# Optimization experiments

Hardware: AMD Instinct MI355X
Metric: run time of the kernel (lower is better)

Reference implementation:

```python
import jax, jax.numpy as jnp
import numpy as np

D = 50          # half-window
K = 2 * D + 1   # 101 window positions
P_SIZE = 100    # predictive-alignment hidden dim


def setup_inputs() -> dict:
    key = jax.random.key(0)
    ks = jax.random.split(key, 5)
    B, S, CQ, CC = 2, 2048, 256, 256
    q = jax.random.normal(ks[0], (B, S, CQ), jnp.float32)
    c_t = jax.random.normal(ks[1], (B, S, CC), jnp.float32)
    W_a = jax.random.normal(ks[2], (CC, CQ), jnp.float32) / np.sqrt(CQ).astype(np.float32)
    W_p = jax.random.normal(ks[3], (P_SIZE, CC), jnp.float32) / np.sqrt(CC).astype(np.float32)
    V_p = jax.random.normal(ks[4], (1, P_SIZE), jnp.float32) / np.sqrt(P_SIZE).astype(np.float32)
    return {"q": q, "c_t": c_t, "W_a": W_a, "W_p": W_p, "V_p": V_p}


def reference(q, c_t, W_a, W_p, V_p):
    B, S, CQ = q.shape
    # predictive alignment: p in (0, S), one predicted center per (b, s)
    p = S * jax.nn.sigmoid(jnp.tanh(c_t @ W_p.T) @ V_p.T)[..., 0]          # [B,S]
    offs = jnp.arange(-D, D + 1)                                           # [K]
    # torch .long() truncates toward zero (raw can be negative)
    raw = jnp.trunc(p[..., None] + offs[None, None, :] + 1.0).astype(jnp.int32)
    # clamp to [0, S+1] then mod (S+1): index 0 == padded (invalid) row,
    # matching torch's NaN-padded row 0 (S+1 wraps to 0 via the modulo)
    idx = jnp.clip(raw, 0, S + 1) % (S + 1)                                # [B,S,K]
    mask = idx == 0                                                        # invalid window slots
    # pad row 0 (torch pads with NaN then zeroes the NaN rows; we pad with 0
    # and mask by index -> identical math for finite q)
    q_pad = jnp.concatenate([jnp.zeros((B, 1, CQ), q.dtype), q], axis=1)   # [B,S+1,CQ]
    gathered = jnp.take_along_axis(q_pad, idx.reshape(B, S * K, 1), axis=1)
    q1 = jnp.where(mask[..., None], 0.0, gathered.reshape(B, S, K, CQ))    # [B,S,K,CQ]
    # score: W_a projection then dot with context
    Wq = jnp.einsum("bskq,cq->bskc", q1, W_a)                              # [B,S,K,CC]
    a = jnp.einsum("bskc,bsc->bsk", Wq, c_t)                               # [B,S,K]
    a = jnp.where(mask, -jnp.inf, a)
    attn = jax.nn.softmax(a, axis=2)                                       # [B,S,K]
    # gaussian decay centered at floor(p) (p > 0 so trunc == floor)
    exponent = -2.0 * (((offs[None, None, :] + jnp.trunc(p)[..., None] - p[..., None]) / D) ** 2)
    w = attn * jnp.exp(exponent)                                           # [B,S,K]
    s_t = jnp.einsum("bsk,bskc->bsc", w, q1)                               # [B,S,CQ]
    return s_t
```

## Files before the change

kernel.cpp:

```cpp
#include <hip/hip_runtime.h>
#include <math.h>

#define S_LEN 2048
#define NB    2
#define CQ_   256
#define CC_   256
#define DH    50
#define KW    101
#define PS    100
#define RB    8
#define HPAD  128
#define WTH   1e-5f

__global__ __launch_bounds__(128) void k_prep(const float* __restrict__ Wp,
                                              float* __restrict__ WpT) {
  const int c = blockIdx.x, j = threadIdx.x;
  WpT[c * HPAD + j] = (j < PS) ? Wp[j * CC_ + c] : 0.0f;
}

__global__ __launch_bounds__(384, 3) void k_align(const float* __restrict__ ct,
    const float* __restrict__ Wa, const float* __restrict__ WpT,
    const float* __restrict__ Vp, float* __restrict__ p_out,
    float* __restrict__ V_out) {
  const int r0  = blockIdx.x * RB;
  const int tid = threadIdx.x;
  const float* crow = ct + (size_t)r0 * CC_;

  __shared__ float red[RB][PS + 4];

  if (tid < CQ_) {
    const float* wa = Wa + tid;
    float acc[RB];
#pragma unroll
    for (int r = 0; r < RB; ++r) acc[r] = 0.0f;

    float4 cv0[RB], cv1[RB];
#pragma unroll
    for (int r = 0; r < RB; ++r) cv0[r] = *(const float4*)&crow[r * CC_];
    float w00 = wa[0 * CQ_], w01 = wa[1 * CQ_], w02 = wa[2 * CQ_], w03 = wa[3 * CQ_];

    for (int c = 0; c < CC_ - 4; c += 4) {
      const int cn = c + 4;
#pragma unroll
      for (int r = 0; r < RB; ++r) cv1[r] = *(const float4*)&crow[r * CC_ + cn];
      const float w10 = wa[(size_t)(cn + 0) * CQ_];
      const float w11 = wa[(size_t)(cn + 1) * CQ_];
      const float w12 = wa[(size_t)(cn + 2) * CQ_];
      const float w13 = wa[(size_t)(cn + 3) * CQ_];
#pragma unroll
      for (int r = 0; r < RB; ++r) {
        float t = acc[r];
        t = fmaf(cv0[r].x, w00, t);
        t = fmaf(cv0[r].y, w01, t);
        t = fmaf(cv0[r].z, w02, t);
        t = fmaf(cv0[r].w, w03, t);
        acc[r] = t;
      }
#pragma unroll
      for (int r = 0; r < RB; ++r) cv0[r] = cv1[r];
      w00 = w10; w01 = w11; w02 = w12; w03 = w13;
    }
#pragma unroll
    for (int r = 0; r < RB; ++r) {
      float t = acc[r];
      t = fmaf(cv0[r].x, w00, t);
      t = fmaf(cv0[r].y, w01, t);
      t = fmaf(cv0[r].z, w02, t);
      t = fmaf(cv0[r].w, w03, t);
      acc[r] = t;
    }
#pragma unroll
    for (int r = 0; r < RB; ++r)
      V_out[(size_t)(r0 + r) * CQ_ + tid] = acc[r];
  } else {
    const int j = tid - CQ_;
    const float* wh = WpT + j;
    float ah[RB];
#pragma unroll
    for (int r = 0; r < RB; ++r) ah[r] = 0.0f;

    float4 cv0[RB], cv1[RB];
#pragma unroll
    for (int r = 0; r < RB; ++r) cv0[r] = *(const float4*)&crow[r * CC_];
    float w00 = wh[0 * HPAD], w01 = wh[1 * HPAD], w02 = wh[2 * HPAD], w03 = wh[3 * HPAD];

    for (int c = 0; c < CC_ - 4; c += 4) {
      const int cn = c + 4;
#pragma unroll
      for (int r = 0; r < RB; ++r) cv1[r] = *(const float4*)&crow[r * CC_ + cn];
      const float w10 = wh[(size_t)(cn + 0) * HPAD];
      const float w11 = wh[(size_t)(cn + 1) * HPAD];
      const float w12 = wh[(size_t)(cn + 2) * HPAD];
      const float w13 = wh[(size_t)(cn + 3) * HPAD];
#pragma unroll
      for (int r = 0; r < RB; ++r) {
        float t = ah[r];
        t = fmaf(cv0[r].x, w00, t);
        t = fmaf(cv0[r].y, w01, t);
        t = fmaf(cv0[r].z, w02, t);
        t = fmaf(cv0[r].w, w03, t);
        ah[r] = t;
      }
#pragma unroll
      for (int r = 0; r < RB; ++r) cv0[r] = cv1[r];
      w00 = w10; w01 = w11; w02 = w12; w03 = w13;
    }
#pragma unroll
    for (int r = 0; r < RB; ++r) {
      float t = ah[r];
      t = fmaf(cv0[r].x, w00, t);
      t = fmaf(cv0[r].y, w01, t);
      t = fmaf(cv0[r].z, w02, t);
      t = fmaf(cv0[r].w, w03, t);
      ah[r] = t;
    }
    if (j < PS) {
      const float vp = Vp[j];
#pragma unroll
      for (int r = 0; r < RB; ++r) red[r][j] = vp * tanhf(ah[r]);
    }
  }
  __syncthreads();
  if (tid < RB) {
    float s = 0.0f;
    for (int j = 0; j < PS; ++j) s += red[tid][j];
    p_out[r0 + tid] = (float)S_LEN * (1.0f / (1.0f + expf(-s)));
  }
}

__global__ __launch_bounds__(256, 4) void k_attn(const float* __restrict__ q,
    const float* __restrict__ p_in, const float* V,
    float* out) {
  const int wid  = threadIdx.x >> 6;
  const int row  = (blockIdx.x << 2) + wid;
  const int lane = threadIdx.x & 63;
  const int b    = row >> 11;

  __shared__ float ss[4][128];
  __shared__ float sw[4][128];

  const float p  = p_in[row];
  const float tp = truncf(p);
  const float* qb = q + (size_t)b * S_LEN * CQ_;

  const int sub = lane >> 4;
  const int cb  = (lane & 15) * 16;

  const float* vrow = V + (size_t)row * CQ_ + cb;
  const float4 v0 = *(const float4*)(vrow);
  const float4 v1 = *(const float4*)(vrow + 4);
  const float4 v2 = *(const float4*)(vrow + 8);
  const float4 v3 = *(const float4*)(vrow + 12);

  if (lane >= KW - 64) ss[wid][64 + lane] = -INFINITY;

  for (int g = 0; g < 26; g += 2) {
    const int ka = (g << 2) + sub;
    const int kb = ka + 4;
    const float ta = p + (float)(ka - DH) + 1.0f;
    const float tb = p + (float)(kb - DH) + 1.0f;
    const int rawa = (int)ta;
    const int rawb = (int)tb;
    const bool oka = (rawa >= 1) && (rawa <= S_LEN) && (ka < KW);
    const bool okb = (rawb >= 1) && (rawb <= S_LEN) && (kb < KW);
    const float* qra = qb + (size_t)(oka ? rawa - 1 : 0) * CQ_ + cb;
    const float* qrb = qb + (size_t)(okb ? rawb - 1 : 0) * CQ_ + cb;

    const float4 a0 = *(const float4*)(qra);
    const float4 a1 = *(const float4*)(qra + 4);
    const float4 a2 = *(const float4*)(qra + 8);
    const float4 a3 = *(const float4*)(qra + 12);
    const float4 b0 = *(const float4*)(qrb);
    const float4 b1 = *(const float4*)(qrb + 4);
    const float4 b2 = *(const float4*)(qrb + 8);
    const float4 b3 = *(const float4*)(qrb + 12);

    float t0 = a0.x * v0.x, t1 = a1.x * v1.x, t2 = a2.x * v2.x, t3 = a3.x * v3.x;
    t0 = fmaf(a0.y, v0.y, t0); t1 = fmaf(a1.y, v1.y, t1);
    t2 = fmaf(a2.y, v2.y, t2); t3 = fmaf(a3.y, v3.y, t3);
    t0 = fmaf(a0.z, v0.z, t0); t1 = fmaf(a1.z, v1.z, t1);
    t2 = fmaf(a2.z, v2.z, t2); t3 = fmaf(a3.z, v3.z, t3);
    t0 = fmaf(a0.w, v0.w, t0); t1 = fmaf(a1.w, v1.w, t1);
    t2 = fmaf(a2.w, v2.w, t2); t3 = fmaf(a3.w, v3.w, t3);
    float sA = (t0 + t1) + (t2 + t3);
    sA += __shfl_xor(sA, 1, 64);
    sA += __shfl_xor(sA, 2, 64);
    sA += __shfl_xor(sA, 4, 64);
    sA += __shfl_xor(sA, 8, 64);
    sA = oka ? sA : -INFINITY;
    if ((lane & 15) == 0) ss[wid][ka] = sA;

    float u0 = b0.x * v0.x, u1 = b1.x * v1.x, u2 = b2.x * v2.x, u3 = b3.x * v3.x;
    u0 = fmaf(b0.y, v0.y, u0); u1 = fmaf(b1.y, v1.y, u1);
    u2 = fmaf(b2.y, v2.y, u2); u3 = fmaf(b3.y, v3.y, u3);
    u0 = fmaf(b0.z, v0.z, u0); u1 = fmaf(b1.z, v1.z, u1);
    u2 = fmaf(b2.z, v2.z, u2); u3 = fmaf(b3.z, v3.z, u3);
    u0 = fmaf(b0.w, v0.w, u0); u1 = fmaf(b1.w, v1.w, u1);
    u2 = fmaf(b2.w, v2.w, u2); u3 = fmaf(b3.w, v3.w, u3);
    float sB = (u0 + u1) + (u2 + u3);
    sB += __shfl_xor(sB, 1, 64);
    sB += __shfl_xor(sB, 2, 64);
    sB += __shfl_xor(sB, 4, 64);
    sB += __shfl_xor(sB, 8, 64);
    sB = okb ? sB : -INFINITY;
    if ((lane & 15) == 0) ss[wid][kb] = sB;
  }

  const float s0 = ss[wid][lane];
  const float s1 = ss[wid][64 + lane];

  float m = fmaxf(s0, s1);
#pragma unroll
  for (int off = 1; off < 64; off <<= 1) m = fmaxf(m, __shfl_xor(m, off, 64));

  const float e0 = __expf(s0 - m);
  const float e1 = __expf(s1 - m);
  float den = e0 + e1;
#pragma unroll
  for (int off = 1; off < 64; off <<= 1) den += __shfl_xor(den, off, 64);
  const float inv = 1.0f / den;

  float g0 = ((float)(lane - DH) + tp - p) / (float)DH;
  float g1 = ((float)(lane + (64 - DH)) + tp - p) / (float)DH;
  const float w0 = e0 * __expf(-2.0f * g0 * g0) * inv;
  const float w1 = e1 * __expf(-2.0f * g1 * g1) * inv;
  sw[wid][lane] = w0;
  if (lane < KW - 64) sw[wid][64 + lane] = w1;

  unsigned long long m0 = __ballot(w0 > WTH);
  unsigned long long m1 = __ballot((lane < KW - 64) && (w1 > WTH));

  float4 acc = make_float4(0.0f, 0.0f, 0.0f, 0.0f);
  while ((m0 | m1) != 0ull) {
    int kk[4];
#pragma unroll
    for (int i = 0; i < 4; ++i) {
      int k = -1;
      if (m0)      { k = __builtin_ctzll(m0);      m0 &= m0 - 1; }
      else if (m1) { k = 64 + __builtin_ctzll(m1); m1 &= m1 - 1; }
      kk[i] = k;
    }
#pragma unroll
    for (int i = 0; i < 4; ++i) {
      if (kk[i] >= 0) {
        const float wk = sw[wid][kk[i]];
        const float t = p + (float)(kk[i] - DH) + 1.0f;
        const int r = (int)t - 1;
        const float4 qv = *(const float4*)(qb + (size_t)r * CQ_ + lane * 4);
        acc.x = fmaf(wk, qv.x, acc.x);
        acc.y = fmaf(wk, qv.y, acc.y);
        acc.z = fmaf(wk, qv.z, acc.z);
        acc.w = fmaf(wk, qv.w, acc.w);
      }
    }
  }
  *(float4*)(out + (size_t)row * CQ_ + lane * 4) = acc;
}

extern "C" void kernel_launch(void* const* d_in, const int* in_sizes, int n_in,
                              void* d_out, int out_size, void* d_ws, size_t ws_size,
                              hipStream_t stream) {
  const float* q  = (const float*)d_in[0];
  const float* ct = (const float*)d_in[1];
  const float* Wa = (const float*)d_in[2];
  const float* Wp = (const float*)d_in[3];
  const float* Vp = (const float*)d_in[4];
  float* out = (float*)d_out;

  float* ws     = (float*)d_ws;
  float* p_ws   = ws;
  float* WpT_ws = ws + NB * S_LEN;

  k_prep <<<CC_, HPAD, 0, stream>>>(Wp, WpT_ws);
  k_align<<<(NB * S_LEN) / RB, 384, 0, stream>>>(ct, Wa, WpT_ws, Vp, p_ws, out);
  k_attn <<<(NB * S_LEN) / 4, 256, 0, stream>>>(q, p_ws, out, out);
}
```

Baseline: 120.1 us.

## Replace row-blocked align kernel with shared-memory tiled GEMM over concatenated weights

Concatenates W_a and W_p into one packed [CC,384] weight matrix and computes c_t times it with a classic 64x64 LDS-tiled SGEMM, writing both the W_a projection and the hidden pre-activations to a workspace buffer. A separate small kernel then applies tanh, the V_p dot and the sigmoid to produce p, and the attention kernel reads its projection from the wider workspace rows. The aim is much better weight reuse than the old per-8-row kernel, which reread the weights from global memory for every block. In exchange it adds an extra kernel launch and a G workspace write/read.

```diff
diff --git a/kernel.cpp b/kernel.cpp
--- a/kernel.cpp
+++ b/kernel.cpp
@@ -8,129 +8,100 @@
 #define DH    50
 #define KW    101
 #define PS    100
-#define RB    8
-#define HPAD  128
 #define WTH   1e-5f
 
-__global__ __launch_bounds__(128) void k_prep(const float* __restrict__ Wp,
-                                              float* __restrict__ WpT) {
-  const int c = blockIdx.x, j = threadIdx.x;
-  WpT[c * HPAD + j] = (j < PS) ? Wp[j * CC_ + c] : 0.0f;
-}
-
-__global__ __launch_bounds__(384, 3) void k_align(const float* __restrict__ ct,
-    const float* __restrict__ Wa, const float* __restrict__ WpT,
-    const float* __restrict__ Vp, float* __restrict__ p_out,
-    float* __restrict__ V_out) {
-  const int r0  = blockIdx.x * RB;
+#define NB2   384
+#define MT    64
+#define NT    64
+#define KC    32
+
+__global__ __launch_bounds__(NB2) void k_prep(const float* __restrict__ Wa,
+    const float* __restrict__ Wp, float* __restrict__ BT) {
+  const int c = blockIdx.x, n = threadIdx.x;
+  float v = 0.0f;
+  if (n < CQ_)            v = Wa[(size_t)c * CQ_ + n];
+  else if (n < CQ_ + PS)  v = Wp[(size_t)(n - CQ_) * CC_ + c];
+  BT[(size_t)c * NB2 + n] = v;
+}
+
+__global__ __launch_bounds__(256) void k_gemm(const float* __restrict__ ct,
+    const float* __restrict__ BT, float* __restrict__ G) {
+  const int bm = blockIdx.x & 63;
+  const int bn = blockIdx.x >> 6;
+  const int r0 = bm * MT;
+  const int n0 = bn * NT;
   const int tid = threadIdx.x;
-  const float* crow = ct + (size_t)r0 * CC_;
-
-  __shared__ float red[RB][PS + 4];
-
-  if (tid < CQ_) {
-    const float* wa = Wa + tid;
-    float acc[RB];
-#pragma unroll
-    for (int r = 0; r < RB; ++r) acc[r] = 0.0f;
-
-    float4 cv0[RB], cv1[RB];
-#pragma unroll
-    for (int r = 0; r < RB; ++r) cv0[r] = *(const float4*)&crow[r * CC_];
-    float w00 = wa[0 * CQ_], w01 = wa[1 * CQ_], w02 = wa[2 * CQ_], w03 = wa[3 * CQ_];
-
-    for (int c = 0; c < CC_ - 4; c += 4) {
-      const int cn = c + 4;
-#pragma unroll
-      for (int r = 0; r < RB; ++r) cv1[r] = *(const float4*)&crow[r * CC_ + cn];
-      const float w10 = wa[(size_t)(cn + 0) * CQ_];
-      const float w11 = wa[(size_t)(cn + 1) * CQ_];
-      const float w12 = wa[(size_t)(cn + 2) * CQ_];
-      const float w13 = wa[(size_t)(cn + 3) * CQ_];
-#pragma unroll
-      for (int r = 0; r < RB; ++r) {
-        float t = acc[r];
-        t = fmaf(cv0[r].x, w00, t);
-        t = fmaf(cv0[r].y, w01, t);
-        t = fmaf(cv0[r].z, w02, t);
-        t = fmaf(cv0[r].w, w03, t);
-        acc[r] = t;
-      }
-#pragma unroll
-      for (int r = 0; r < RB; ++r) cv0[r] = cv1[r];
-      w00 = w10; w01 = w11; w02 = w12; w03 = w13;
+  const int tx = tid & 15, ty = tid >> 4;
+
+  __shared__ float As[KC][MT + 4];
+  __shared__ float Bs[KC][NT + 4];
+
+  float acc[4][4];
+#pragma unroll
+  for (int i = 0; i < 4; ++i)
+#pragma unroll
+    for (int j = 0; j < 4; ++j) acc[i][j] = 0.0f;
+
+  const int kq = tid & 7,  mA = tid >> 3;
+  const int nq = tid & 15, kB = tid >> 4;
+
+  for (int c0 = 0; c0 < CC_; c0 += KC) {
+    const float4 a0 = *(const float4*)&ct[(size_t)(r0 + mA) * CC_ + c0 + kq * 4];
+    const float4 a1 = *(const float4*)&ct[(size_t)(r0 + mA + 32) * CC_ + c0 + kq * 4];
+    const float4 b0 = *(const float4*)&BT[(size_t)(c0 + kB) * NB2 + n0 + nq * 4];
+    const float4 b1 = *(const float4*)&BT[(size_t)(c0 + kB + 16) * NB2 + n0 + nq * 4];
+    __syncthreads();
+    As[kq * 4 + 0][mA] = a0.x;
+    As[kq * 4 + 1][mA] = a0.y;
+    As[kq * 4 + 2][mA] = a0.z;
+    As[kq * 4 + 3][mA] = a0.w;
+    As[kq * 4 + 0][mA + 32] = a1.x;
+    As[kq * 4 + 1][mA + 32] = a1.y;
+    As[kq * 4 + 2][mA + 32] = a1.z;
+    As[kq * 4 + 3][mA + 32] = a1.w;
+    *(float4*)&Bs[kB][nq * 4]      = b0;
+    *(float4*)&Bs[kB + 16][nq * 4] = b1;
+    __syncthreads();
+#pragma unroll
+    for (int k = 0; k < KC; ++k) {
+      const float4 av = *(const float4*)&As[k][ty * 4];
+      const float4 bv = *(const float4*)&Bs[k][tx * 4];
+      const float a[4] = {av.x, av.y, av.z, av.w};
+      const float b[4] = {bv.x, bv.y, bv.z, bv.w};
+#pragma unroll
+      for (int i = 0; i < 4; ++i)
+#pragma unroll
+        for (int j = 0; j < 4; ++j) acc[i][j] = fmaf(a[i], b[j], acc[i][j]);
     }
-#pragma unroll
-    for (int r = 0; r < RB; ++r) {
-      float t = acc[r];
-      t = fmaf(cv0[r].x, w00, t);
-      t = fmaf(cv0[r].y, w01, t);
-      t = fmaf(cv0[r].z, w02, t);
-      t = fmaf(cv0[r].w, w03, t);
-      acc[r] = t;
-    }
-#pragma unroll
-    for (int r = 0; r < RB; ++r)
-      V_out[(size_t)(r0 + r) * CQ_ + tid] = acc[r];
-  } else {
-    const int j = tid - CQ_;
-    const float* wh = WpT + j;
-    float ah[RB];
-#pragma unroll
-    for (int r = 0; r < RB; ++r) ah[r] = 0.0f;
-
-    float4 cv0[RB], cv1[RB];
-#pragma unroll
-    for (int r = 0; r < RB; ++r) cv0[r] = *(const float4*)&crow[r * CC_];
-    float w00 = wh[0 * HPAD], w01 = wh[1 * HPAD], w02 = wh[2 * HPAD], w03 = wh[3 * HPAD];
-
-    for (int c = 0; c < CC_ - 4; c += 4) {
-      const int cn = c + 4;
-#pragma unroll
-      for (int r = 0; r < RB; ++r) cv1[r] = *(const float4*)&crow[r * CC_ + cn];
-      const float w10 = wh[(size_t)(cn + 0) * HPAD];
-      const float w11 = wh[(size_t)(cn + 1) * HPAD];
-      const float w12 = wh[(size_t)(cn + 2) * HPAD];
-      const float w13 = wh[(size_t)(cn + 3) * HPAD];
-#pragma unroll
-      for (int r = 0; r < RB; ++r) {
-        float t = ah[r];
-        t = fmaf(cv0[r].x, w00, t);
-        t = fmaf(cv0[r].y, w01, t);
-        t = fmaf(cv0[r].z, w02, t);
-        t = fmaf(cv0[r].w, w03, t);
-        ah[r] = t;
-      }
-#pragma unroll
-      for (int r = 0; r < RB; ++r) cv0[r] = cv1[r];
-      w00 = w10; w01 = w11; w02 = w12; w03 = w13;
-    }
-#pragma unroll
-    for (int r = 0; r < RB; ++r) {
-      float t = ah[r];
-      t = fmaf(cv0[r].x, w00, t);
-      t = fmaf(cv0[r].y, w01, t);
-      t = fmaf(cv0[r].z, w02, t);
-      t = fmaf(cv0[r].w, w03, t);
-      ah[r] = t;
-    }
-    if (j < PS) {
-      const float vp = Vp[j];
-#pragma unroll
-      for (int r = 0; r < RB; ++r) red[r][j] = vp * tanhf(ah[r]);
-    }
-  }
-  __syncthreads();
-  if (tid < RB) {
-    float s = 0.0f;
-    for (int j = 0; j < PS; ++j) s += red[tid][j];
-    p_out[r0 + tid] = (float)S_LEN * (1.0f / (1.0f + expf(-s)));
-  }
+  }
+
+#pragma unroll
+  for (int i = 0; i < 4; ++i) {
+    float4 o;
+    o.x = acc[i][0]; o.y = acc[i][1]; o.z = acc[i][2]; o.w = acc[i][3];
+    *(float4*)&G[(size_t)(r0 + ty * 4 + i) * NB2 + n0 + tx * 4] = o;
+  }
+}
+
+__global__ __launch_bounds__(256) void k_p(const float* __restrict__ G,
+    const float* __restrict__ Vp, float* __restrict__ p_out) {
+  const int r = blockIdx.x * 256 + threadIdx.x;
+  const float* h = G + (size_t)r * NB2 + CQ_;
+  float H[PS];
+#pragma unroll
+  for (int j = 0; j < PS; j += 4) {
+    const float4 v = *(const float4*)&h[j];
+    H[j + 0] = v.x; H[j + 1] = v.y; H[j + 2] = v.z; H[j + 3] = v.w;
+  }
+  float s = 0.0f;
+#pragma unroll
+  for (int j = 0; j < PS; ++j) s += Vp[j] * tanhf(H[j]);
+  p_out[r] = (float)S_LEN * (1.0f / (1.0f + expf(-s)));
 }
 
 __global__ __launch_bounds__(256, 4) void k_attn(const float* __restrict__ q,
-    const float* __restrict__ p_in, const float* V,
-    float* out) {
+    const float* __restrict__ p_in, const float* __restrict__ G,
+    float* __restrict__ out) {
   const int wid  = threadIdx.x >> 6;
   const int row  = (blockIdx.x << 2) + wid;
   const int lane = threadIdx.x & 63;
@@ -146,7 +117,7 @@
   const int sub = lane >> 4;
   const int cb  = (lane & 15) * 16;
 
-  const float* vrow = V + (size_t)row * CQ_ + cb;
+  const float* vrow = G + (size_t)row * NB2 + cb;
   const float4 v0 = *(const float4*)(vrow);
   const float4 v1 = *(const float4*)(vrow + 4);
   const float4 v2 = *(const float4*)(vrow + 8);
@@ -267,11 +238,13 @@
   const float* Vp = (const float*)d_in[4];
   float* out = (float*)d_out;
 
-  float* ws     = (float*)d_ws;
-  float* p_ws   = ws;
-  float* WpT_ws = ws + NB * S_LEN;
-
-  k_prep <<<CC_, HPAD, 0, stream>>>(Wp, WpT_ws);
-  k_align<<<(NB * S_LEN) / RB, 384, 0, stream>>>(ct, Wa, WpT_ws, Vp, p_ws, out);
-  k_attn <<<(NB * S_LEN) / 4, 256, 0, stream>>>(q, p_ws, out, out);
-}
+  float* ws    = (float*)d_ws;
+  float* p_ws  = ws;
+  float* BT_ws = ws + NB * S_LEN;
+  float* G_ws  = BT_ws + (size_t)CC_ * NB2;
+
+  k_prep<<<CC_, NB2, 0, stream>>>(Wa, Wp, BT_ws);
+  k_gemm<<<64 * 6, 256, 0, stream>>>(ct, BT_ws, G_ws);
+  k_p   <<<(NB * S_LEN) / 256, 256, 0, stream>>>(G_ws, Vp, p_ws);
+  k_attn<<<(NB * S_LEN) / 4, 256, 0, stream>>>(q, p_ws, G_ws, out);
+}
```

Measured after the change: 125.4 us. 4.4% more time.
